# Performance work log

Measured on AMD Instinct MI355X. Metric: run time of the kernel, lower is better.

The kernel has to match this reference:

```python
import jax, jax.numpy as jnp
import numpy as np

H = 256
NUM_REL = 460
NUM_ENT = 20000
B = 4096
CUR_TS = 10
PATH_LEN = 8


def _gru_step(x, h, W_ih, W_hh, b_ih, b_hh):
    # PyTorch GRUCell math
    gi = x @ W_ih.T + b_ih          # [B, 3H]
    gh = h @ W_hh.T + b_hh          # [B, 3H]
    ir, iz, inn = jnp.split(gi, 3, axis=1)
    hr, hz, hn = jnp.split(gh, 3, axis=1)
    r = jax.nn.sigmoid(ir + hr)
    z = jax.nn.sigmoid(iz + hz)
    n = jnp.tanh(inn + r * hn)
    return (1.0 - z) * n + z * h


def setup_inputs() -> dict:
    key = jax.random.key(0)
    ks = jax.random.split(key, 24)
    s = 1.0 / np.sqrt(H)
    f32 = jnp.float32
    d = {
        "pre_emb": jax.random.normal(ks[0], (NUM_ENT, H), f32),
        "r_emb": jax.random.normal(ks[1], (NUM_REL, H), f32),
        "partial_embeding": jax.random.normal(ks[2], (B, CUR_TS * NUM_REL), f32),
        # params (uniform-ish linear init scaled by 1/sqrt(H))
        "W_map1": jax.random.normal(ks[3], (2 * H, H), f32) * s,
        "b_map1": jax.random.normal(ks[4], (2 * H,), f32) * s,
        "W_map2": jax.random.normal(ks[5], (H, 2 * H), f32) * s,
        "b_map2": jax.random.normal(ks[6], (H,), f32) * s,
        "W_h1": jax.random.normal(ks[7], (H, H), f32) * s,
        "b_h1": jax.random.normal(ks[8], (H,), f32) * s,
        "W_h2": jax.random.normal(ks[9], (H, H), f32) * s,
        "b_h2": jax.random.normal(ks[10], (H,), f32) * s,
        "W_attn": jax.random.normal(ks[11], (H, H), f32) * s,
        "b_attn": jax.random.normal(ks[12], (H,), f32) * s,
        "W_align": jax.random.normal(ks[13], (H, H), f32) * s,
        "b_align": jax.random.normal(ks[14], (H,), f32) * s,
        "W_ih": jax.random.normal(ks[15], (3 * H, H), f32) * s,
        "W_hh": jax.random.normal(ks[16], (3 * H, H), f32) * s,
        "b_ih": jax.random.normal(ks[17], (3 * H,), f32) * s,
        "b_hh": jax.random.normal(ks[18], (3 * H,), f32) * s,
        "all_triples": jax.random.randint(ks[19], (B, 3), 0, NUM_REL, dtype=jnp.int64)
        if jax.config.jax_enable_x64 else jax.random.randint(ks[19], (B, 3), 0, NUM_REL, dtype=jnp.int32),
        "cur_ts": CUR_TS,
        "num_rel": NUM_REL,
    }
    return d


def reference(pre_emb, r_emb, partial_embeding,
              W_map1, b_map1, W_map2, b_map2,
              W_h1, b_h1, W_h2, b_h2,
              W_attn, b_attn, W_align, b_align,
              W_ih, W_hh, b_ih, b_hh,
              all_triples, cur_ts, num_rel):
    # rel_mapping1 -> rel_mapping2
    mapped_rel = (r_emb @ W_map1.T + b_map1) @ W_map2.T + b_map2     # [R, H]
    q_rel = mapped_rel[all_triples[:, 1]]                            # [B, H]

    # attention logits base (constant over timesteps): linear_attn(q_rel) @ mapped_rel.T
    attn_base = (q_rel @ W_attn.T + b_attn) @ mapped_rel.T           # [B, R]

    start_ts = max(cur_ts - PATH_LEN, 0)
    nb = partial_embeding.shape[0]
    cur_seq = partial_embeding.reshape(nb, cur_ts, num_rel)[:, start_ts:cur_ts]  # [B, T, R]
    cur_seq = jnp.swapaxes(cur_seq, 0, 1)                            # [T, B, R]

    h0 = jnp.zeros((nb, H), dtype=pre_emb.dtype)

    def step(h, cur):
        attn = cur * attn_base
        attn = jnp.where(attn == 0, jnp.asarray(-1e9, attn.dtype), attn)
        attn = jax.nn.softmax(attn, axis=1)
        x = attn @ mapped_rel                                        # [B, H]
        return _gru_step(x, h, W_ih, W_hh, b_ih, b_hh), None

    gru_hidden, _ = jax.lax.scan(step, h0, cur_seq)

    # predicted history embedding + match loss (MSE)
    predicted_hist = 0.1 * ((q_rel @ W_h1.T + b_h1) @ W_h2.T + b_h2) + q_rel
    match_loss = jnp.mean((predicted_hist - gru_hidden) ** 2)

    # forward_forth, distmult scoring
    h2 = _gru_step(q_rel, predicted_hist, W_ih, W_hh, b_ih, b_hh)    # [B, H]
    aligned_all = pre_emb @ W_align.T + b_align                      # [E, H]
    sub = aligned_all[all_triples[:, 0]]                             # [B, H]
    score_logits = (sub * h2) @ aligned_all.T                        # [B, E]
    score = jax.nn.sigmoid(score_logits)

    # BCE(sigmoid(logits), one_hot(obj)) in stable logits form without
    # materializing the dense one-hot label matrix:
    # mean over B*E of [ softplus(x) - x * label ]
    obj = all_triples[:, 2]
    pos_logits = score_logits[jnp.arange(nb), obj]
    path_loss = (jnp.sum(jax.nn.softplus(score_logits)) - jnp.sum(pos_logits)) / (nb * score_logits.shape[1])

    return match_loss, path_loss, score
```

## Files before the change

kernel.cpp:

```cpp
#include <hip/hip_runtime.h>
#include <hip/hip_bf16.h>

typedef __hip_bfloat16 bf16;
typedef __attribute__((ext_vector_type(8))) short short8;
typedef __attribute__((ext_vector_type(4))) float f32x4;
typedef __attribute__((ext_vector_type(4))) short short4v;

#define NREL 460
#define KP   480
#define NENT 20000
#define NENT_PAD 20224
#define NB   4096

__device__ inline float sigmoidf_(float x){ return 1.f/(1.f+__expf(-x)); }

__device__ inline void gload16(const bf16* g, bf16* l){
  __builtin_amdgcn_global_load_lds(
      (const __attribute__((address_space(1))) unsigned int*)g,
      (__attribute__((address_space(3))) unsigned int*)l, 16, 0, 0);
}

__device__ __forceinline__ void fgemm_body(
    const float* __restrict__ A, int lda, int arows,
    const float* __restrict__ B, int ldb,
    const float* __restrict__ bias,
    float* __restrict__ C, int ldc, int K, int mode,
    const float* __restrict__ add_src, bf16* __restrict__ ct_out,
    float* As, float* Bs, int bx, int by)
{
  const int tid = threadIdx.x;
  const int row0 = bx*64, col0 = by*64;
  const int tx = tid & 15, ty = tid >> 4;
  float acc[4][4] = {};
  for (int k0 = 0; k0 < K; k0 += 32){
    __syncthreads();
    #pragma unroll
    for (int s = 0; s < 2; ++s){
      int slot = tid + s*256;
      int r = slot >> 3, c4 = (slot & 7)*4;
      int ra = row0 + r; if (ra >= arows) ra = arows - 1;
      float4 v = *(const float4*)(A + (long)ra*lda + k0 + c4);
      As[(c4+0)*68+r] = v.x; As[(c4+1)*68+r] = v.y; As[(c4+2)*68+r] = v.z; As[(c4+3)*68+r] = v.w;
      float4 w = *(const float4*)(B + (long)(col0 + r)*ldb + k0 + c4);
      Bs[(c4+0)*68+r] = w.x; Bs[(c4+1)*68+r] = w.y; Bs[(c4+2)*68+r] = w.z; Bs[(c4+3)*68+r] = w.w;
    }
    __syncthreads();
    #pragma unroll
    for (int kk = 0; kk < 32; ++kk){
      float4 a4 = *(const float4*)(&As[kk*68 + ty*4]);
      float4 b4 = *(const float4*)(&Bs[kk*68 + tx*4]);
      float av[4] = {a4.x, a4.y, a4.z, a4.w};
      float bv[4] = {b4.x, b4.y, b4.z, b4.w};
      #pragma unroll
      for (int i = 0; i < 4; ++i)
        #pragma unroll
        for (int j = 0; j < 4; ++j) acc[i][j] += av[i]*bv[j];
    }
  }
  const int rb = row0 + ty*4, cb = col0 + tx*4;
  if (mode == 1){
    #pragma unroll
    for (int i = 0; i < 4; ++i){
      float4 v = {acc[i][0], acc[i][1], acc[i][2], acc[i][3]};
      *(float4*)(C + (long)(rb+i)*ldc + cb) = v;
      int rr = rb + i;
      if (rr < KP){
        #pragma unroll
        for (int j = 0; j < 4; ++j)
          ct_out[(cb+j)*KP + rr] = __float2bfloat16(rr < NREL ? acc[i][j] : 0.f);
      }
    }
  } else if (mode == 2){
    #pragma unroll
    for (int i = 0; i < 4; ++i){
      float4 v;
      #pragma unroll
      for (int j = 0; j < 4; ++j)
        ((float*)&v)[j] = 0.1f*(acc[i][j] + bias[cb+j]) + add_src[(long)(rb+i)*ldc + cb+j];
      *(float4*)(C + (long)(rb+i)*ldc + cb) = v;
    }
  } else {
    float bv[4] = {0,0,0,0};
    if (bias){ bv[0]=bias[cb]; bv[1]=bias[cb+1]; bv[2]=bias[cb+2]; bv[3]=bias[cb+3]; }
    #pragma unroll
    for (int i = 0; i < 4; ++i){
      float4 v = {acc[i][0]+bv[0], acc[i][1]+bv[1], acc[i][2]+bv[2], acc[i][3]+bv[3]};
      *(float4*)(C + (long)(rb+i)*ldc + cb) = v;
    }
  }
}

struct FDesc {
  const float* A; const float* B; const float* bias; float* C;
  const float* add; bf16* ct;
  int lda, ldb, ldc, K, arows, mode;
};

__device__ __forceinline__ void gemm128_body1(
    const bf16* __restrict__ A, int lda,
    const bf16* __restrict__ B, int ldb,
    const float* __restrict__ bias,
    bf16* __restrict__ C, long ldc, int K,
    bf16* sbuf, int bx, int by)
{
  const int tid = threadIdx.x;
  const int lane = tid & 63, wave = tid >> 6;
  const long row0 = (long)bx * 128;
  const long col0 = (long)by * 128;
  const int sr = tid >> 2;
  const int sc = ((tid & 3) ^ ((sr >> 1) & 3)) * 8;
  const bf16* Ag0 = A + (row0 + sr)*lda + sc;
  const bf16* Ag1 = A + (row0 + 64 + sr)*lda + sc;
  const bf16* Bg0 = B + (col0 + sr)*ldb + sc;
  const bf16* Bg1 = B + (col0 + 64 + sr)*ldb + sc;
  bf16* As_ = sbuf;
  bf16* Bs_ = sbuf + 8192;
  const int wr = (wave >> 1)*64, wc = (wave & 1)*64;
  const int rA = lane & 15;
  const int kA = ((lane >> 4) ^ ((rA >> 1) & 3)) * 8;
  f32x4 acc[4][4] = {};
  const int nt = K >> 5;
  gload16(Ag0, As_ + tid*8);
  gload16(Ag1, As_ + 2048 + tid*8);
  gload16(Bg0, Bs_ + tid*8);
  gload16(Bg1, Bs_ + 2048 + tid*8);
  int cur = 0;
  for (int t = 0; t < nt; ++t){
    if (t + 1 < nt){
      const int k0 = (t+1) << 5;
      const int nxt = cur ^ 1;
      gload16(Ag0 + k0, As_ + nxt*4096 + tid*8);
      gload16(Ag1 + k0, As_ + nxt*4096 + 2048 + tid*8);
      gload16(Bg0 + k0, Bs_ + nxt*4096 + tid*8);
      gload16(Bg1 + k0, Bs_ + nxt*4096 + 2048 + tid*8);
      asm volatile("s_waitcnt vmcnt(4)" ::: "memory");
    } else {
      asm volatile("s_waitcnt vmcnt(0)" ::: "memory");
    }
    __builtin_amdgcn_s_barrier();
    short8 a[4], b[4];
    #pragma unroll
    for (int m = 0; m < 4; ++m) a[m] = *(const short8*)(As_ + cur*4096 + (wr + m*16 + rA)*32 + kA);
    #pragma unroll
    for (int n = 0; n < 4; ++n) b[n] = *(const short8*)(Bs_ + cur*4096 + (wc + n*16 + rA)*32 + kA);
    asm volatile("s_waitcnt lgkmcnt(0)" ::: "memory");
    __builtin_amdgcn_s_barrier();
    #pragma unroll
    for (int m = 0; m < 4; ++m)
      #pragma unroll
      for (int n = 0; n < 4; ++n)
        acc[m][n] = __builtin_amdgcn_mfma_f32_16x16x32_bf16(a[m], b[n], acc[m][n], 0,0,0);
    cur ^= 1;
  }
  const int ri = (lane >> 4)*4, ci = lane & 15;
  __syncthreads();
  bf16* epi = sbuf + wave*1152;
  const int rrow = lane >> 2, q = lane & 3;
  #pragma unroll
  for (int m = 0; m < 4; ++m){
    #pragma unroll
    for (int n = 0; n < 4; ++n){
      long c = col0 + wc + n*16 + ci;
      float bv = bias ? bias[c] : 0.f;
      #pragma unroll
      for (int i = 0; i < 4; ++i)
        epi[(ri+i)*72 + n*16 + ci] = __float2bfloat16(acc[m][n][i] + bv);
    }
    long gr = row0 + wr + m*16 + rrow;
    bf16* gp = C + gr*ldc + col0 + wc + q*16;
    const bf16* lp = epi + rrow*72 + q*16;
    *(short8*)(gp)     = *(const short8*)(lp);
    *(short8*)(gp + 8) = *(const short8*)(lp + 8);
  }
}

template<int MODE>
__device__ __forceinline__ void gemm512_body(
    const bf16* __restrict__ A, int lda,
    const bf16* __restrict__ B, int ldb,
    const float* __restrict__ bias,
    void* __restrict__ C, long ldc,
    int K, int n_valid, double* __restrict__ sp_sum,
    const int* __restrict__ trips,
    bf16* sbuf, float* wsum, int bx, int by)
{
  const int tid = threadIdx.x;
  const int lane = tid & 63, wave = tid >> 6;
  const long row0 = (long)bx * 128;
  const long col0 = (long)by * 128;
  const int sr = tid >> 2;
  const int sc = ((tid & 3) ^ ((sr >> 1) & 3)) * 8;
  const bf16* Ag = A + (row0 + sr)*lda + sc;
  const bf16* Bg = B + (col0 + sr)*ldb + sc;
  bf16* As_ = sbuf;
  bf16* Bs_ = sbuf + 8192;
  const int wr = (wave >> 2)*64, wc = (wave & 3)*32;
  const int rA = lane & 15;
  const int kA = ((lane >> 4) ^ ((rA >> 1) & 3)) * 8;
  f32x4 acc[4][2] = {};
  const int nt = K >> 5;
  gload16(Ag, As_ + tid*8);
  gload16(Bg, Bs_ + tid*8);
  int cur = 0;
  for (int t = 0; t < nt; ++t){
    if (t + 1 < nt){
      const int k0 = (t+1) << 5;
      const int nxt = cur ^ 1;
      gload16(Ag + k0, As_ + nxt*4096 + tid*8);
      gload16(Bg + k0, Bs_ + nxt*4096 + tid*8);
      asm volatile("s_waitcnt vmcnt(2)" ::: "memory");
    } else {
      asm volatile("s_waitcnt vmcnt(0)" ::: "memory");
    }
    __builtin_amdgcn_s_barrier();
    short8 a[4], b[2];
    #pragma unroll
    for (int m = 0; m < 4; ++m) a[m] = *(const short8*)(As_ + cur*4096 + (wr + m*16 + rA)*32 + kA);
    #pragma unroll
    for (int n = 0; n < 2; ++n) b[n] = *(const short8*)(Bs_ + cur*4096 + (wc + n*16 + rA)*32 + kA);
    asm volatile("s_waitcnt lgkmcnt(0)" ::: "memory");
    __builtin_amdgcn_s_barrier();
    #pragma unroll
    for (int m = 0; m < 4; ++m)
      #pragma unroll
      for (int n = 0; n < 2; ++n)
        acc[m][n] = __builtin_amdgcn_mfma_f32_16x16x32_bf16(a[m], b[n], acc[m][n], 0,0,0);
    cur ^= 1;
  }
  const int ri = (lane >> 4)*4, ci = lane & 15;
  __syncthreads();
  if constexpr (MODE == 1){
    bf16* epi = sbuf + wave*640;
    const int rw = lane >> 2, q = lane & 3;
    #pragma unroll
    for (int m = 0; m < 4; ++m){
      #pragma unroll
      for (int n = 0; n < 2; ++n){
        long c = col0 + wc + n*16 + ci;
        float bv = bias ? bias[c] : 0.f;
        #pragma unroll
        for (int i = 0; i < 4; ++i)
          epi[(ri+i)*40 + n*16 + ci] = __float2bfloat16(acc[m][n][i] + bv);
      }
      long gr = row0 + wr + m*16 + rw;
      bf16* gp = (bf16*)C + gr*ldc + col0 + wc + q*8;
      *(short8*)(gp) = *(const short8*)(epi + rw*40 + q*8);
    }
  } else {
    float* epi = (float*)sbuf + wave*576;
    const int rw = lane >> 2, q = lane & 3;
    const bool maybe = (col0 + wc) < 464;
    float spart = 0.f, ppart = 0.f;
    #pragma unroll
    for (int m = 0; m < 4; ++m){
      int obj[4];
      if (maybe){
        #pragma unroll
        for (int i = 0; i < 4; ++i)
          obj[i] = trips[3*(int)(row0 + wr + m*16 + ri + i) + 2];
      }
      #pragma unroll
      for (int n = 0; n < 2; ++n){
        long c = col0 + wc + n*16 + ci;
        bool cv = (c < n_valid);
        #pragma unroll
        for (int i = 0; i < 4; ++i){
          float v = acc[m][n][i];
          float sg = 0.f;
          if (cv){
            float e = __expf(-fabsf(v));
            float tt = 1.f + e;
            float rr = __builtin_amdgcn_rcpf(tt);
            sg = (v >= 0.f) ? rr : 1.f - rr;
            spart += fmaxf(v, 0.f) + e*(0.9404f - 0.2537f*e);
            if (maybe && c == obj[i]) ppart += v;
          }
          epi[(ri+i)*36 + n*16 + ci + 2] = sg;
        }
      }
      long gr = row0 + wr + m*16 + rw;
      long c8 = col0 + wc + q*8;
      if (c8 < n_valid){
        float* gp = (float*)C + gr*ldc + c8;
        const float* lp = epi + rw*36 + q*8 + 2;
        *(float2*)(gp)     = *(const float2*)(lp);
        *(float4*)(gp + 2) = *(const float4*)(lp + 2);
        *(float2*)(gp + 6) = *(const float2*)(lp + 6);
      }
    }
    #pragma unroll
    for (int off = 32; off >= 1; off >>= 1){
      spart += __shfl_xor(spart, off);
      ppart += __shfl_xor(ppart, off);
    }
    if (lane == 0){ wsum[wave] = spart; wsum[8+wave] = ppart; }
    __syncthreads();
    if (tid == 0){
      float s = 0.f;
      #pragma unroll
      for (int w = 0; w < 8; ++w) s += wsum[w];
      atomicAdd(sp_sum, (double)s);
    }
    if (tid == 1){
      float p = 0.f;
      #pragma unroll
      for (int w = 0; w < 8; ++w) p += wsum[8+w];
      atomicAdd(sp_sum+1, (double)p);
    }
  }
}

__global__ __launch_bounds__(256) void k_conv_g1(
    const float4* __restrict__ s0, short4v* __restrict__ d0, int n0,
    const float4* __restrict__ s1, short4v* __restrict__ d1, int n1,
    const float4* __restrict__ s2, short4v* __restrict__ d2, int n2,
    short4v* __restrict__ pad0, int n3, double* __restrict__ dz,
    const float* __restrict__ gA, const float* __restrict__ gB,
    const float* __restrict__ gbias, float* __restrict__ gC)
{
  __shared__ __align__(16) float As[32*68];
  __shared__ __align__(16) float Bs[32*68];
  int bid = blockIdx.x;
  if (bid < 64){
    fgemm_body(gA,256,NREL, gB,256, gbias, gC,512, 256, 0, nullptr,nullptr,
               As, Bs, bid&7, bid>>3);
    return;
  }
  int i = (bid-64)*256 + threadIdx.x;
  if (i < n0+n1+n2){
    const float4* s; short4v* d; int j;
    if (i < n0){ s = s0; d = d0; j = i; }
    else if (i < n0+n1){ s = s1; d = d1; j = i-n0; }
    else { s = s2; d = d2; j = i-n0-n1; }
    float4 v = s[j];
    bf16 a = __float2bfloat16(v.x), b = __float2bfloat16(v.y);
    bf16 c = __float2bfloat16(v.z), e = __float2bfloat16(v.w);
    short4v o; o.x = *(short*)&a; o.y = *(short*)&b; o.z = *(short*)&c; o.w = *(short*)&e;
    d[j] = o;
  } else if (i < n0+n1+n2+n3){
    short4v z = {0,0,0,0};
    pad0[i - (n0+n1+n2)] = z;
  } else if (i < n0+n1+n2+n3+8){
    dz[i - (n0+n1+n2+n3)] = 0.0;
  }
}

__global__ __launch_bounds__(256) void k_fgemm(
    const float* A, int lda, int arows, const float* B, int ldb,
    const float* bias, float* C, int ldc, int K, int mode,
    const float* add_src, bf16* ct_out){
  __shared__ __align__(16) float As[32*68];
  __shared__ __align__(16) float Bs[32*68];
  fgemm_body(A, lda, arows, B, ldb, bias, C, ldc, K, mode, add_src, ct_out,
             As, Bs, blockIdx.x, blockIdx.y);
}

__global__ __launch_bounds__(256) void k_fgemm_multi(FDesc d0, FDesc d1, FDesc d2,
                                                     int y1, int y2){
  __shared__ __align__(16) float As[32*68];
  __shared__ __align__(16) float Bs[32*68];
  int y = blockIdx.y;
  FDesc d; int by;
  if (y < y1){ d = d0; by = y; }
  else if (y < y2){ d = d1; by = y - y1; }
  else { d = d2; by = y - y2; }
  fgemm_body(d.A, d.lda, d.arows, d.B, d.ldb, d.bias, d.C, d.ldc, d.K, d.mode,
             d.add, d.ct, As, Bs, blockIdx.x, by);
}

__global__ __launch_bounds__(256) void k_g3_aligned(
    FDesc d0, FDesc d1, FDesc d2, int y1, int y2,
    const bf16* __restrict__ pA, const bf16* __restrict__ pB,
    const float* __restrict__ pbias, bf16* __restrict__ pC)
{
  __shared__ __align__(16) char smem[34816];
  int bid = blockIdx.x;
  if (bid < 160){
    int bx = bid & 7, y = bid >> 3;
    FDesc d; int by;
    if (y < y1){ d = d0; by = y; }
    else if (y < y2){ d = d1; by = y - y1; }
    else { d = d2; by = y - y2; }
    fgemm_body(d.A, d.lda, d.arows, d.B, d.ldb, d.bias, d.C, d.ldc, d.K, d.mode,
               d.add, d.ct, (float*)smem, (float*)(smem + 17408), bx, by);
  } else {
    int idx = bid - 160;
    gemm128_body1(pA, 256, pB, 256, pbias, pC, 256, 256,
                  (bf16*)smem, idx % 158, idx / 158);
  }
}

__global__ __launch_bounds__(256) void k_soft_makep(const float* __restrict__ partial,
    const float* __restrict__ attn_base, const int* __restrict__ trips,
    bf16* __restrict__ attn_all,
    const bf16* __restrict__ Qbf,
    const float* __restrict__ M_ih, const float* __restrict__ ghp,
    const float* __restrict__ ph, const float* __restrict__ b_ih,
    bf16* __restrict__ P){
  int bid = blockIdx.x;
  if (bid >= NB/4){
    int i = (bid - NB/4)*256 + threadIdx.x;
    int b = i >> 8, k = i & 255;
    int s = trips[b*3+0], rel = trips[b*3+1];
    long rb = (long)rel*768;
    float rg = sigmoidf_(M_ih[rb+k]     + b_ih[k]     + ghp[rb+k]);
    float zg = sigmoidf_(M_ih[rb+256+k] + b_ih[256+k] + ghp[rb+256+k]);
    float ng = tanhf    (M_ih[rb+512+k] + b_ih[512+k] + rg*ghp[rb+512+k]);
    float h2v = (1.f - zg)*ng + zg*ph[rel*256+k];
    P[i] = __float2bfloat16(__bfloat162float(Qbf[(long)s*256+k]) * h2v);
    return;
  }
  int wave = threadIdx.x >> 6, lane = threadIdx.x & 63;
  int b = bid*4 + wave;
  int rel = trips[b*3+1];
  const float* base = attn_base + (long)rel*512;
  float bs[8];
  #pragma unroll
  for (int s = 0; s < 8; ++s){
    int idx = s*64 + lane;
    bs[s] = (idx < NREL) ? base[idx] : 0.f;
  }
  const float* cur0 = partial + (long)b*4600 + 2*NREL;
  for (int t = 0; t < 8; ++t){
    const float* cur = cur0 + t*NREL;
    float v[8]; float mx = -1e30f;
    #pragma unroll
    for (int s = 0; s < 8; ++s){
      int idx = s*64 + lane;
      float val = -1e30f;
      if (idx < NREL){
        float pz = cur[idx]*bs[s];
        val = (pz == 0.f) ? -1e9f : pz;
      }
      v[s] = val; mx = fmaxf(mx, val);
    }
    #pragma unroll
    for (int off = 32; off >= 1; off >>= 1) mx = fmaxf(mx, __shfl_xor(mx, off));
    float sum = 0.f;
    #pragma unroll
    for (int s = 0; s < 8; ++s){
      int idx = s*64 + lane;
      if (idx < NREL){ v[s] = __expf(v[s]-mx); sum += v[s]; }
    }
    #pragma unroll
    for (int off = 32; off >= 1; off >>= 1) sum += __shfl_xor(sum, off);
    float inv = 1.f/sum;
    long obase = ((long)t*NB + b)*KP;
    #pragma unroll
    for (int s = 0; s < 8; ++s){
      int idx = s*64 + lane;
      if (idx < KP) attn_all[obase + idx] = __float2bfloat16(idx < NREL ? v[s]*inv : 0.f);
    }
  }
}

__global__ __launch_bounds__(512, 4) void k_gemm_dual(
    const bf16* __restrict__ A2, const bf16* __restrict__ B2,
    void* __restrict__ C2, long ldc2, int K2, int nvalid2,
    double* __restrict__ sp, const int* __restrict__ trips, int nblk2,
    const bf16* __restrict__ A1, const bf16* __restrict__ B1,
    const float* __restrict__ bias1, void* __restrict__ C1, long ldc1, int K1)
{
  __shared__ __align__(16) bf16 sbuf[16384];
  __shared__ float wsum[16];
  int bid = blockIdx.x;
  if (bid < nblk2){
    gemm512_body<2>(A2, 256, B2, 256, nullptr, C2, ldc2, K2, nvalid2, sp, trips,
                    sbuf, wsum, bid & 31, bid >> 5);
  } else {
    int idx = bid - nblk2;
    gemm512_body<1>(A1, KP, B1, KP, bias1, C1, ldc1, K1, 0, nullptr, nullptr,
                    sbuf, wsum, idx & 255, idx >> 8);
  }
}

__global__ __launch_bounds__(512) void k_scan(
    const bf16* __restrict__ gi_all,
    const bf16* __restrict__ W_hh_bf,
    const float* __restrict__ b_hh,
    const float* __restrict__ ph,
    const int* __restrict__ trips,
    double* __restrict__ dsum, int* __restrict__ done, float* __restrict__ outf)
{
  __shared__ __align__(16) bf16 hl[16*264];
  __shared__ __align__(16) bf16 gbuf[2][16*768];
  __shared__ float red[8];
  const int tid = threadIdx.x;
  const int lane = tid & 63, wave = tid >> 6;
  const int brow0 = blockIdx.x * 16;
  const int rA = lane & 15, kA = (lane >> 4) * 8;
  const int ci = lane & 15, rbase = (lane >> 4) * 4;
  float hreg[2][4] = {};
  float bh[3][2];
  #pragma unroll
  for (int f = 0; f < 2; ++f){
    int cf = wave*32 + f*16 + ci;
    bh[0][f] = b_hh[cf]; bh[1][f] = b_hh[256+cf]; bh[2][f] = b_hh[512+cf];
  }
  short8 warr[3][2][6];
  #pragma unroll
  for (int g = 0; g < 3; ++g)
    #pragma unroll
    for (int f = 0; f < 2; ++f)
      #pragma unroll
      for (int k = 0; k < 6; ++k)
        warr[g][f][k] = *(const short8*)(W_hh_bf + (g*256 + wave*32 + f*16 + rA)*256 + k*32 + kA);
  {
    const bf16* src = gi_all + (long)brow0 * 768;
    #pragma unroll
    for (int i = 0; i < 3; ++i){
      int off = (wave*3 + i)*512 + lane*8;
      gload16(src + off, gbuf[0] + off);
    }
  }
  int cur = 0;
  for (int t = 0; t < 8; ++t){
    f32x4 acc[3][2] = {};
    if (t > 0){
      #pragma unroll
      for (int k = 0; k < 8; ++k){
        short8 a = *(const short8*)(hl + rA*264 + k*32 + kA);
        #pragma unroll
        for (int g = 0; g < 3; ++g)
          #pragma unroll
          for (int f = 0; f < 2; ++f){
            short8 b;
            if (k < 6) b = warr[g][f][k];
            else b = *(const short8*)(W_hh_bf + (g*256 + wave*32 + f*16 + rA)*256 + k*32 + kA);
            acc[g][f] = __builtin_amdgcn_mfma_f32_16x16x32_bf16(a, b, acc[g][f], 0,0,0);
          }
      }
    }
    asm volatile("s_waitcnt lgkmcnt(0) vmcnt(0)" ::: "memory");
    __builtin_amdgcn_s_barrier();
    if (t < 7){
      const bf16* src = gi_all + ((long)(t+1)*NB + brow0) * 768;
      bf16* dst = gbuf[cur ^ 1];
      #pragma unroll
      for (int i = 0; i < 3; ++i){
        int off = (wave*3 + i)*512 + lane*8;
        gload16(src + off, dst + off);
      }
    }
    const bf16* gl = gbuf[cur];
    #pragma unroll
    for (int f = 0; f < 2; ++f){
      int cf = wave*32 + f*16 + ci;
      #pragma unroll
      for (int i = 0; i < 4; ++i){
        int rloc = rbase + i;
        float gir = __bfloat162float(gl[rloc*768 + cf]);
        float giz = __bfloat162float(gl[rloc*768 + 256 + cf]);
        float gin = __bfloat162float(gl[rloc*768 + 512 + cf]);
        float rg = sigmoidf_(gir + acc[0][f][i] + bh[0][f]);
        float zg = sigmoidf_(giz + acc[1][f][i] + bh[1][f]);
        float ng = tanhf(gin + rg*(acc[2][f][i] + bh[2][f]));
        float hn = (1.f - zg)*ng + zg*hreg[f][i];
        hreg[f][i] = hn;
        hl[rloc*264 + cf] = __float2bfloat16(hn);
      }
    }
    asm volatile("s_waitcnt lgkmcnt(0)" ::: "memory");
    __builtin_amdgcn_s_barrier();
    cur ^= 1;
  }
  float d = 0.f;
  #pragma unroll
  for (int f = 0; f < 2; ++f){
    int cf = wave*32 + f*16 + ci;
    #pragma unroll
    for (int i = 0; i < 4; ++i){
      int rel = trips[(brow0 + rbase + i)*3 + 1];
      float diff = ph[rel*256 + cf] - hreg[f][i];
      d += diff*diff;
    }
  }
  #pragma unroll
  for (int off = 32; off >= 1; off >>= 1) d += __shfl_xor(d, off);
  if (lane == 0) red[wave] = d;
  __syncthreads();
  if (tid == 0){
    float s = 0.f;
    #pragma unroll
    for (int w = 0; w < 8; ++w) s += red[w];
    atomicAdd(dsum, (double)s);
    asm volatile("s_waitcnt vmcnt(0)" ::: "memory");
    int ticket = atomicAdd(done, 1);
    if (ticket == (int)gridDim.x - 1){
      double m  = atomicAdd(dsum+0, 0.0);
      double sp = atomicAdd(dsum+1, 0.0);
      double pp = atomicAdd(dsum+2, 0.0);
      outf[0] = (float)(m / (4096.0*256.0));
      outf[1] = (float)((sp - pp) / (4096.0*20000.0));
    }
  }
}

extern "C" void kernel_launch(void* const* d_in, const int* in_sizes, int n_in,
                              void* d_out, int out_size, void* d_ws, size_t ws_size,
                              hipStream_t stream){
  const float* pre_emb = (const float*)d_in[0];
  const float* r_emb   = (const float*)d_in[1];
  const float* partial = (const float*)d_in[2];
  const float* W_map1  = (const float*)d_in[3];
  const float* b_map1  = (const float*)d_in[4];
  const float* W_map2  = (const float*)d_in[5];
  const float* b_map2  = (const float*)d_in[6];
  const float* W_h1    = (const float*)d_in[7];
  const float* b_h1    = (const float*)d_in[8];
  const float* W_h2    = (const float*)d_in[9];
  const float* b_h2    = (const float*)d_in[10];
  const float* W_attn  = (const float*)d_in[11];
  const float* b_attn  = (const float*)d_in[12];
  const float* W_align = (const float*)d_in[13];
  const float* b_align = (const float*)d_in[14];
  const float* W_ih    = (const float*)d_in[15];
  const float* W_hh    = (const float*)d_in[16];
  const float* b_ih    = (const float*)d_in[17];
  const float* b_hh    = (const float*)d_in[18];
  const int*   trips   = (const int*)d_in[19];
  float* out = (float*)d_out;

  char* w = (char*)d_ws;
  auto alloc = [&](size_t bytes)->char*{
    char* r = w; w += (bytes + 255) & ~size_t(255); return r;
  };
  double* dsum      = (double*)alloc(128);
  int*    done      = (int*)(dsum + 4);
  float* t1         = (float*)alloc(512*512*4);
  float* mapped     = (float*)alloc(512*256*4);
  float* a1         = (float*)alloc(512*256*4);
  float* th         = (float*)alloc(512*256*4);
  float* ph         = (float*)alloc(512*256*4);
  float* M_ih       = (float*)alloc(512*768*4);
  float* ghp        = (float*)alloc(512*768*4);
  float* attn_base  = (float*)alloc(512*512*4);
  bf16*  M_ihT      = (bf16*)alloc(768*KP*2);
  bf16*  W_hh_bf    = (bf16*)alloc(768*256*2);
  bf16*  W_align_bf = (bf16*)alloc(256*256*2);
  bf16*  Q_bf       = (bf16*)alloc((size_t)NENT_PAD*256*2);
  bf16*  P_bf       = (bf16*)alloc((size_t)NB*256*2);
  bf16*  attn_all   = (bf16*)alloc((size_t)8*NB*KP*2);
  bf16*  gi_all     = (bf16*)alloc((size_t)8*NB*768*2);
  bf16*  pre_bf     = attn_all;

  {
    int n0 = NENT*256/4, n1 = 768*256/4, n2 = 256*256/4;
    int n3 = (NENT_PAD-NENT)*256/4;
    int ntot = n0+n1+n2+n3+8;
    k_conv_g1<<<64 + (ntot+255)/256, 256, 0, stream>>>(
        (const float4*)pre_emb, (short4v*)pre_bf, n0,
        (const float4*)W_hh, (short4v*)W_hh_bf, n1,
        (const float4*)W_align, (short4v*)W_align_bf, n2,
        (short4v*)(pre_bf + (size_t)NENT*256), n3, dsum,
        r_emb, W_map1, b_map1, t1);
  }
  k_fgemm<<<dim3(8,4),256,0,stream>>>(t1,512,512, W_map2,512, b_map2, mapped,256, 512, 0, nullptr, nullptr);
  {
    FDesc d0 = { mapped, W_ih,   nullptr, M_ih, nullptr, M_ihT, 256, 256, 768, 256, 512, 1 };
    FDesc d1 = { mapped, W_attn, b_attn,  a1,   nullptr, nullptr, 256, 256, 256, 256, 512, 0 };
    FDesc d2 = { mapped, W_h1,   b_h1,    th,   nullptr, nullptr, 256, 256, 256, 256, 512, 0 };
    k_g3_aligned<<<160 + 316, 256, 0, stream>>>(d0, d1, d2, 12, 16,
                                                pre_bf, W_align_bf, b_align, Q_bf);
  }
  {
    FDesc d0 = { th, W_h2,   b_h2,    ph,        mapped,  nullptr, 256, 256, 256, 256, 512, 2 };
    FDesc d1 = { a1, mapped, nullptr, attn_base, nullptr, nullptr, 256, 256, 512, 256, 512, 0 };
    k_fgemm_multi<<<dim3(8,12),256,0,stream>>>(d0, d1, d1, 4, 12);
  }
  k_fgemm<<<dim3(8,12),256,0,stream>>>(ph,256,512, W_hh,256, b_hh, ghp,768, 256, 0, nullptr, nullptr);
  k_soft_makep<<<NB/4 + NB,256,0,stream>>>(partial, attn_base, trips, attn_all,
                                           Q_bf, M_ih, ghp, ph, b_ih, P_bf);
  k_gemm_dual<<<5056 + 1536, 512, 0, stream>>>(
      P_bf, Q_bf, out+2, NENT, 256, NENT, dsum+1, trips, 5056,
      attn_all, M_ihT, b_ih, gi_all, 768, KP);
  k_scan<<<NB/16,512,0,stream>>>(gi_all, W_hh_bf, b_hh, ph, trips, dsum, done, out);
}
```

Before: 358.4 us.

## Retile score GEMM to 64x256 blocks with dedicated specialized body

Replaces the templated 128x128 score GEMM tile with a specialized 64x256 tile (K=256 fully unrolled, 8 stages) in which each wave computes 32x64 and more B columns are staged per block. The gi GEMM path keeps the old 128x128 body, split into its own function. The wider tile writes 16-float contiguous chunks per lane and reads the fused epilogue data with the same per-block logic. LDS use grows to 40KB, which may reduce occupancy, and the score part now has 5056 blocks of a different shape.

Result: slower. 404.5 us (+12.8%).

```diff
diff --git a/kernel.cpp b/kernel.cpp
--- a/kernel.cpp
+++ b/kernel.cpp
@@ -174,15 +174,12 @@
   }
 }
 
-template<int MODE>
-__device__ __forceinline__ void gemm512_body(
+__device__ __forceinline__ void gemm512_gi(
     const bf16* __restrict__ A, int lda,
     const bf16* __restrict__ B, int ldb,
     const float* __restrict__ bias,
-    void* __restrict__ C, long ldc,
-    int K, int n_valid, double* __restrict__ sp_sum,
-    const int* __restrict__ trips,
-    bf16* sbuf, float* wsum, int bx, int by)
+    bf16* __restrict__ C, long ldc, int K,
+    bf16* sbuf, int bx, int by)
 {
   const int tid = threadIdx.x;
   const int lane = tid & 63, wave = tid >> 6;
@@ -229,84 +226,142 @@
   }
   const int ri = (lane >> 4)*4, ci = lane & 15;
   __syncthreads();
-  if constexpr (MODE == 1){
-    bf16* epi = sbuf + wave*640;
-    const int rw = lane >> 2, q = lane & 3;
-    #pragma unroll
-    for (int m = 0; m < 4; ++m){
-      #pragma unroll
-      for (int n = 0; n < 2; ++n){
-        long c = col0 + wc + n*16 + ci;
-        float bv = bias ? bias[c] : 0.f;
-        #pragma unroll
-        for (int i = 0; i < 4; ++i)
-          epi[(ri+i)*40 + n*16 + ci] = __float2bfloat16(acc[m][n][i] + bv);
+  bf16* epi = sbuf + wave*640;
+  const int rw = lane >> 2, q = lane & 3;
+  #pragma unroll
+  for (int m = 0; m < 4; ++m){
+    #pragma unroll
+    for (int n = 0; n < 2; ++n){
+      long c = col0 + wc + n*16 + ci;
+      float bv = bias ? bias[c] : 0.f;
+      #pragma unroll
+      for (int i = 0; i < 4; ++i)
+        epi[(ri+i)*40 + n*16 + ci] = __float2bfloat16(acc[m][n][i] + bv);
+    }
+    long gr = row0 + wr + m*16 + rw;
+    bf16* gp = C + gr*ldc + col0 + wc + q*8;
+    *(short8*)(gp) = *(const short8*)(epi + rw*40 + q*8);
+  }
+}
+
+__device__ __forceinline__ void score64_body(
+    const bf16* __restrict__ A,
+    const bf16* __restrict__ B,
+    float* __restrict__ C, long ldc, int n_valid,
+    double* __restrict__ sp_sum, const int* __restrict__ trips,
+    bf16* sbuf, float* wsum, int bx, int by)
+{
+  const int tid = threadIdx.x;
+  const int lane = tid & 63, wave = tid >> 6;
+  const long row0 = (long)bx * 64;
+  const long col0 = (long)by * 256;
+  bf16* As_ = sbuf;
+  bf16* Bs_ = sbuf + 4096;
+  const int arow = tid >> 2, ag = tid & 3;
+  const bf16* Ag = A + (row0 + arow)*256 + ((ag ^ ((arow >> 1) & 3)) << 3);
+  const int brow0_ = tid >> 2, bg0 = tid & 3;
+  const int brow1_ = (tid + 512) >> 2, bg1 = tid & 3;
+  const bf16* Bg0 = B + (col0 + brow0_)*256 + ((bg0 ^ ((brow0_ >> 1) & 3)) << 3);
+  const bf16* Bg1 = B + (col0 + brow1_)*256 + ((bg1 ^ ((brow1_ >> 1) & 3)) << 3);
+  const int wr = (wave >> 2)*32, wc = (wave & 3)*64;
+  const int rA = lane & 15;
+  const int kA = ((lane >> 4) ^ ((rA >> 1) & 3)) * 8;
+  f32x4 acc[2][4] = {};
+  auto stage = [&](int k0, int buf){
+    if (tid < 256) gload16(Ag + k0, As_ + buf*2048 + tid*8);
+    gload16(Bg0 + k0, Bs_ + buf*8192 + tid*8);
+    gload16(Bg1 + k0, Bs_ + buf*8192 + 4096 + tid*8);
+  };
+  stage(0, 0);
+  int cur = 0;
+  #pragma unroll
+  for (int t = 0; t < 8; ++t){
+    if (t + 1 < 8){
+      stage((t+1) << 5, cur ^ 1);
+      if (tid < 256) asm volatile("s_waitcnt vmcnt(3)" ::: "memory");
+      else           asm volatile("s_waitcnt vmcnt(2)" ::: "memory");
+    } else {
+      asm volatile("s_waitcnt vmcnt(0)" ::: "memory");
+    }
+    __builtin_amdgcn_s_barrier();
+    short8 a[2], b[4];
+    #pragma unroll
+    for (int m = 0; m < 2; ++m) a[m] = *(const short8*)(As_ + cur*2048 + (wr + m*16 + rA)*32 + kA);
+    #pragma unroll
+    for (int n = 0; n < 4; ++n) b[n] = *(const short8*)(Bs_ + cur*8192 + (wc + n*16 + rA)*32 + kA);
+    asm volatile("s_waitcnt lgkmcnt(0)" ::: "memory");
+    __builtin_amdgcn_s_barrier();
+    #pragma unroll
+    for (int m = 0; m < 2; ++m)
+      #pragma unroll
+      for (int n = 0; n < 4; ++n)
+        acc[m][n] = __builtin_amdgcn_mfma_f32_16x16x32_bf16(a[m], b[n], acc[m][n], 0,0,0);
+    cur ^= 1;
+  }
+  const int ri = (lane >> 4)*4, ci = lane & 15;
+  __syncthreads();
+  float* epi = (float*)sbuf + wave*1088;
+  const int rw = lane >> 2, q = lane & 3;
+  const bool maybe = (col0 + wc) < 464;
+  float spart = 0.f, ppart = 0.f;
+  #pragma unroll
+  for (int m = 0; m < 2; ++m){
+    int obj[4];
+    if (maybe){
+      #pragma unroll
+      for (int i = 0; i < 4; ++i)
+        obj[i] = trips[3*(int)(row0 + wr + m*16 + ri + i) + 2];
+    }
+    #pragma unroll
+    for (int n = 0; n < 4; ++n){
+      long c = col0 + wc + n*16 + ci;
+      bool cv = (c < n_valid);
+      #pragma unroll
+      for (int i = 0; i < 4; ++i){
+        float v = acc[m][n][i];
+        float sg = 0.f;
+        if (cv){
+          float e = __expf(-fabsf(v));
+          float tt = 1.f + e;
+          float rr = __builtin_amdgcn_rcpf(tt);
+          sg = (v >= 0.f) ? rr : 1.f - rr;
+          spart += fmaxf(v, 0.f) + e*(0.9404f - 0.2537f*e);
+          if (maybe && c == obj[i]) ppart += v;
+        }
+        epi[(ri+i)*68 + n*16 + ci + 2] = sg;
       }
-      long gr = row0 + wr + m*16 + rw;
-      bf16* gp = (bf16*)C + gr*ldc + col0 + wc + q*8;
-      *(short8*)(gp) = *(const short8*)(epi + rw*40 + q*8);
-    }
-  } else {
-    float* epi = (float*)sbuf + wave*576;
-    const int rw = lane >> 2, q = lane & 3;
-    const bool maybe = (col0 + wc) < 464;
-    float spart = 0.f, ppart = 0.f;
-    #pragma unroll
-    for (int m = 0; m < 4; ++m){
-      int obj[4];
-      if (maybe){
-        #pragma unroll
-        for (int i = 0; i < 4; ++i)
-          obj[i] = trips[3*(int)(row0 + wr + m*16 + ri + i) + 2];
-      }
-      #pragma unroll
-      for (int n = 0; n < 2; ++n){
-        long c = col0 + wc + n*16 + ci;
-        bool cv = (c < n_valid);
-        #pragma unroll
-        for (int i = 0; i < 4; ++i){
-          float v = acc[m][n][i];
-          float sg = 0.f;
-          if (cv){
-            float e = __expf(-fabsf(v));
-            float tt = 1.f + e;
-            float rr = __builtin_amdgcn_rcpf(tt);
-            sg = (v >= 0.f) ? rr : 1.f - rr;
-            spart += fmaxf(v, 0.f) + e*(0.9404f - 0.2537f*e);
-            if (maybe && c == obj[i]) ppart += v;
-          }
-          epi[(ri+i)*36 + n*16 + ci + 2] = sg;
-        }
-      }
-      long gr = row0 + wr + m*16 + rw;
-      long c8 = col0 + wc + q*8;
-      if (c8 < n_valid){
-        float* gp = (float*)C + gr*ldc + c8;
-        const float* lp = epi + rw*36 + q*8 + 2;
-        *(float2*)(gp)     = *(const float2*)(lp);
-        *(float4*)(gp + 2) = *(const float4*)(lp + 2);
-        *(float2*)(gp + 6) = *(const float2*)(lp + 6);
-      }
-    }
-    #pragma unroll
-    for (int off = 32; off >= 1; off >>= 1){
-      spart += __shfl_xor(spart, off);
-      ppart += __shfl_xor(ppart, off);
-    }
-    if (lane == 0){ wsum[wave] = spart; wsum[8+wave] = ppart; }
+    }
+    long gr = row0 + wr + m*16 + rw;
+    long c16 = col0 + wc + q*16;
+    if (c16 < n_valid){
+      float* gp = C + gr*ldc + c16;
+      const float* lp = epi + rw*68 + q*16 + 2;
+      *(float2*)(gp)      = *(const float2*)(lp);
+      *(float4*)(gp + 2)  = *(const float4*)(lp + 2);
+      *(float4*)(gp + 6)  = *(const float4*)(lp + 6);
+      *(float4*)(gp + 10) = *(const float4*)(lp + 10);
+      *(float2*)(gp + 14) = *(const float2*)(lp + 14);
+    }
     __syncthreads();
-    if (tid == 0){
-      float s = 0.f;
-      #pragma unroll
-      for (int w = 0; w < 8; ++w) s += wsum[w];
-      atomicAdd(sp_sum, (double)s);
-    }
-    if (tid == 1){
-      float p = 0.f;
-      #pragma unroll
-      for (int w = 0; w < 8; ++w) p += wsum[8+w];
-      atomicAdd(sp_sum+1, (double)p);
-    }
+  }
+  #pragma unroll
+  for (int off = 32; off >= 1; off >>= 1){
+    spart += __shfl_xor(spart, off);
+    ppart += __shfl_xor(ppart, off);
+  }
+  if (lane == 0){ wsum[wave] = spart; wsum[8+wave] = ppart; }
+  __syncthreads();
+  if (tid == 0){
+    float s = 0.f;
+    #pragma unroll
+    for (int w = 0; w < 8; ++w) s += wsum[w];
+    atomicAdd(sp_sum, (double)s);
+  }
+  if (tid == 1){
+    float p = 0.f;
+    #pragma unroll
+    for (int w = 0; w < 8; ++w) p += wsum[8+w];
+    atomicAdd(sp_sum+1, (double)p);
   }
 }
 
@@ -456,21 +511,21 @@
 
 __global__ __launch_bounds__(512, 4) void k_gemm_dual(
     const bf16* __restrict__ A2, const bf16* __restrict__ B2,
-    void* __restrict__ C2, long ldc2, int K2, int nvalid2,
+    void* __restrict__ C2, long ldc2, int nvalid2,
     double* __restrict__ sp, const int* __restrict__ trips, int nblk2,
     const bf16* __restrict__ A1, const bf16* __restrict__ B1,
     const float* __restrict__ bias1, void* __restrict__ C1, long ldc1, int K1)
 {
-  __shared__ __align__(16) bf16 sbuf[16384];
+  __shared__ __align__(16) bf16 sbuf[20480];
   __shared__ float wsum[16];
   int bid = blockIdx.x;
   if (bid < nblk2){
-    gemm512_body<2>(A2, 256, B2, 256, nullptr, C2, ldc2, K2, nvalid2, sp, trips,
-                    sbuf, wsum, bid & 31, bid >> 5);
+    score64_body(A2, B2, (float*)C2, ldc2, nvalid2, sp, trips,
+                 sbuf, wsum, bid & 63, bid >> 6);
   } else {
     int idx = bid - nblk2;
-    gemm512_body<1>(A1, KP, B1, KP, bias1, C1, ldc1, K1, 0, nullptr, nullptr,
-                    sbuf, wsum, idx & 255, idx >> 8);
+    gemm512_gi(A1, KP, B1, KP, bias1, (bf16*)C1, ldc1, K1,
+               sbuf, idx & 255, idx >> 8);
   }
 }
 
@@ -671,8 +726,8 @@
   k_fgemm<<<dim3(8,12),256,0,stream>>>(ph,256,512, W_hh,256, b_hh, ghp,768, 256, 0, nullptr, nullptr);
   k_soft_makep<<<NB/4 + NB,256,0,stream>>>(partial, attn_base, trips, attn_all,
                                            Q_bf, M_ih, ghp, ph, b_ih, P_bf);
-  k_gemm_dual<<<5056 + 1536, 512, 0, stream>>>(
-      P_bf, Q_bf, out+2, NENT, 256, NENT, dsum+1, trips, 5056,
+  k_gemm_dual<<<64*79 + 1536, 512, 0, stream>>>(
+      P_bf, Q_bf, out+2, NENT, NENT, dsum+1, trips, 64*79,
       attn_all, M_ihT, b_ih, gi_all, 768, KP);
   k_scan<<<NB/16,512,0,stream>>>(gi_all, W_hh_bf, b_hh, ph, trips, dsum, done, out);
 }
```
